# Optimization experiments

Hardware: AMD Instinct MI355X
Metric: run time of the kernel (lower is better)

The kernel has to match this reference:

```python
import jax, jax.numpy as jnp
import numpy as np

B, S, H, E, I, K = 1, 4096, 1024, 16, 512, 2
ISH = 1024  # shared expert intermediate = moe_intermediate_size * num_shared_experts
ROUTE_SCALE = 1.0
WSCALE = 0.02


def setup_inputs() -> dict:
    key = jax.random.key(0)
    ks = jax.random.split(key, 9)
    return {
        "hidden_states": jax.random.normal(ks[0], (B, S, H), dtype=jnp.float32),
        "router_w": jax.random.normal(ks[1], (H, E), dtype=jnp.float32) * WSCALE,
        "expert_bias": jnp.zeros((E,), dtype=jnp.float32),
        "w_gate": jax.random.normal(ks[2], (E, H, I), dtype=jnp.float32) * WSCALE,
        "w_up": jax.random.normal(ks[3], (E, H, I), dtype=jnp.float32) * WSCALE,
        "w_down": jax.random.normal(ks[4], (E, I, H), dtype=jnp.float32) * WSCALE,
        "sw_gate": jax.random.normal(ks[5], (H, ISH), dtype=jnp.float32) * WSCALE,
        "sw_up": jax.random.normal(ks[6], (H, ISH), dtype=jnp.float32) * WSCALE,
        "sw_down": jax.random.normal(ks[7], (ISH, H), dtype=jnp.float32) * WSCALE,
    }


def reference(hidden_states, router_w, expert_bias, w_gate, w_up, w_down, sw_gate, sw_up, sw_down):
    b, s, h = hidden_states.shape
    T = b * s
    xf = hidden_states.reshape(T, h)

    # --- token-choice router (sigmoid scores, top-k, normalize, scale) ---
    scores = jax.nn.sigmoid((xf @ router_w).astype(jnp.float32))          # [T, E]
    _, sel = jax.lax.top_k(scores + expert_bias[None, :], K)              # [T, K] int32
    top = jnp.take_along_axis(scores, sel, axis=1)                        # [T, K]
    top = top / (top.sum(axis=-1, keepdims=True) + 1e-20)
    top = top * ROUTE_SCALE

    # combine weights: [T, E], zero for unselected experts
    comb = jnp.zeros((T, E), jnp.float32).at[jnp.arange(T)[:, None], sel].add(top)

    # --- routed experts: SwiGLU MLP per expert (stacked weights) ---
    g = jnp.einsum('th,ehi->eti', xf, w_gate)                             # [E, T, I]
    u = jnp.einsum('th,ehi->eti', xf, w_up)                               # [E, T, I]
    a = jax.nn.silu(g) * u                                                # [E, T, I]
    eo = jnp.einsum('eti,eih->eth', a, w_down)                            # [E, T, H]
    routed = jnp.einsum('eth,te->th', eo.astype(jnp.float32), comb).astype(hidden_states.dtype)

    # --- shared experts (always active) ---
    shared = (jax.nn.silu(xf @ sw_gate) * (xf @ sw_up)) @ sw_down         # [T, H]

    return (shared + routed).reshape(b, s, h)
```

## Files before the change

kernel.cpp:

```cpp
#include <hip/hip_runtime.h>
#include <math.h>

#define T_TOK 4096
#define HDIM  1024
#define NEXP  16
#define IDIM  512
#define NSLOT 16384
#define NGRP  18
#define MAXRB 160

typedef unsigned int u32;
typedef unsigned short u16;
typedef __attribute__((ext_vector_type(8))) short bfrag;
typedef __attribute__((ext_vector_type(4))) float f32x4;

__device__ __forceinline__ u16 f2bf(float f) {
    union { float f; u32 u; } c; c.f = f;
    u32 u = c.u;
    u32 r = u + 0x7fffu + ((u >> 16) & 1u);
    return (u16)(r >> 16);
}
__device__ __forceinline__ float bf2f(u16 h) {
    union { u32 u; float f; } c; c.u = ((u32)h) << 16;
    return c.f;
}

__device__ __forceinline__ void async16(void* lds, const void* g) {
    __builtin_amdgcn_global_load_lds((__attribute__((address_space(1))) void*)(g),
                                     (__attribute__((address_space(3))) void*)(lds),
                                     16, 0, 0);
}

__global__ __launch_bounds__(256) void cvt_f32_bf16(const float* __restrict__ src,
                                                    u16* __restrict__ dst, int n) {
    int i = (blockIdx.x * 256 + threadIdx.x) * 4;
    if (i >= n) return;
    float4 v = *(const float4*)(src + i);
    ushort4 o;
    o.x = f2bf(v.x); o.y = f2bf(v.y); o.z = f2bf(v.z); o.w = f2bf(v.w);
    *(ushort4*)(dst + i) = o;
}

__global__ __launch_bounds__(256) void transpose_k(const float* __restrict__ src,
                                                   u16* __restrict__ dst,
                                                   int R, int C, long bstride) {
    __shared__ float tile[32][33];
    long base = (long)blockIdx.z * bstride;
    int c0 = blockIdx.x * 32, r0 = blockIdx.y * 32;
    int tx = threadIdx.x, ty = threadIdx.y;
#pragma unroll
    for (int j = 0; j < 4; ++j)
        tile[ty + 8 * j][tx] = src[base + (long)(r0 + ty + 8 * j) * C + (c0 + tx)];
    __syncthreads();
#pragma unroll
    for (int j = 0; j < 4; ++j)
        dst[base + (long)(c0 + ty + 8 * j) * R + (r0 + tx)] = f2bf(tile[tx][ty + 8 * j]);
}

__global__ __launch_bounds__(256) void router_k(const float* __restrict__ x,
                                                const float* __restrict__ rw,
                                                const float* __restrict__ bias,
                                                int* __restrict__ sel,
                                                float* __restrict__ wts) {
    int tid = threadIdx.x;
    int wv = tid >> 6;
    int lane = tid & 63;
    int t = blockIdx.x * 4 + wv;
    int e = lane & 15, hc = lane >> 4;
    const float* xr = x + (long)t * HDIM + hc * 256;
    const float* rp = rw + (long)hc * 256 * NEXP + e;
    float acc = 0.f;
#pragma unroll 4
    for (int i = 0; i < 64; ++i) {
        float4 xv = *(const float4*)(xr + i * 4);
        acc += xv.x * rp[(i * 4 + 0) * NEXP] + xv.y * rp[(i * 4 + 1) * NEXP]
             + xv.z * rp[(i * 4 + 2) * NEXP] + xv.w * rp[(i * 4 + 3) * NEXP];
    }
    acc += __shfl_down(acc, 16);
    acc += __shfl_down(acc, 32);
    float sc = 1.f / (1.f + __expf(-acc));
    float v = sc + bias[e];
    int i0 = -1, i1 = -1;
    float v0 = -1e30f, v1 = -1e30f, s0 = 0.f, s1 = 0.f;
#pragma unroll
    for (int j = 0; j < 16; ++j) {
        float vj = __shfl(v, j);
        float scj = __shfl(sc, j);
        if (vj > v0) { v1 = v0; i1 = i0; s1 = s0; v0 = vj; i0 = j; s0 = scj; }
        else if (vj > v1) { v1 = vj; i1 = j; s1 = scj; }
    }
    if (lane == 0) {
        float nrm = s0 + s1 + 1e-20f;
        sel[t * 2] = i0; sel[t * 2 + 1] = i1;
        wts[t * 2] = s0 / nrm; wts[t * 2 + 1] = s1 / nrm;
    }
}

__global__ __launch_bounds__(1024) void route_build_k(const int* __restrict__ sel,
                                                      int* __restrict__ offs,
                                                      int* __restrict__ rowmap,
                                                      int* __restrict__ invmap,
                                                      int* __restrict__ rbGroup,
                                                      int* __restrict__ rbRow0) {
    __shared__ int hist[NEXP];
    __shared__ int cur[NEXP];
    int tid = threadIdx.x;
    if (tid < NEXP) hist[tid] = 0;
    __syncthreads();
    for (int i = tid; i < T_TOK * 2; i += 1024)
        atomicAdd(&hist[sel[i]], 1);
    __syncthreads();
    if (tid == 0) {
        int a = 0;
        for (int g = 0; g < NEXP; ++g) { cur[g] = a; offs[g] = a; a += hist[g]; }
        offs[16] = 8192;
        offs[17] = 8192 + T_TOK;
        offs[18] = 8192 + 2 * T_TOK;
        int rb = 0;
        for (int g = 0; g < NGRP; ++g)
            for (int r0 = offs[g]; r0 < offs[g + 1]; r0 += 128) {
                rbGroup[rb] = g; rbRow0[rb] = r0; ++rb;
            }
        for (; rb < MAXRB; ++rb) rbGroup[rb] = -1;
    }
    __syncthreads();
    for (int i = tid; i < T_TOK * 2; i += 1024) {
        int g = sel[i];
        int slot = atomicAdd(&cur[g], 1);
        rowmap[slot] = i >> 1;
        invmap[i] = slot;
    }
    for (int i = tid; i < T_TOK; i += 1024) {
        rowmap[8192 + i] = i;
        rowmap[8192 + T_TOK + i] = i;
    }
}

__global__ __launch_bounds__(256)
void gemm_gu(const u16* __restrict__ A,
             const u16* __restrict__ WG,
             const u16* __restrict__ WU,
             const u16* __restrict__ SWG,
             const u16* __restrict__ SWU,
             u16* __restrict__ H,
             const int* __restrict__ offs,
             const int* __restrict__ rowmap,
             const int* __restrict__ rbGroup,
             const int* __restrict__ rbRow0) {
    int rb = blockIdx.y;
    int g = rbGroup[rb];
    if (g < 0) return;
    int row0 = rbRow0[rb];
    int mend = offs[g + 1];
    int col0 = blockIdx.x * 64;
    long wb = (long)((g < 16) ? g : (g - 16)) * IDIM * HDIM;
    const u16* Bg = (g < 16) ? WG + wb : SWG + wb;
    const u16* Bu = (g < 16) ? WU + wb : SWU + wb;

    __shared__ u16 sA[128 * 64];
    __shared__ u16 sBg[64 * 64];
    __shared__ u16 sBu[64 * 64];

    int tid = threadIdx.x;
    int lane = tid & 63;
    int w = tid >> 6;
    int wr = (w >> 1) * 64, wc = (w & 1) * 32;
    int lhi = lane >> 4, llo = lane & 15;
    int swz = llo & 7;

    const u16* pA[4]; u16* dA[4];
#pragma unroll
    for (int c = 0; c < 4; ++c) {
        int idx = c * 256 + tid;
        int r = idx >> 3, ch = idx & 7;
        int grow = row0 + r;
        int ar = rowmap[(grow < mend) ? grow : row0];
        pA[c] = A + (long)ar * HDIM + ((ch ^ (r & 7)) * 8);
        dA[c] = &sA[idx * 8];
    }
    const u16* pBg[2]; const u16* pBu[2]; u16* dBg[2]; u16* dBu[2];
#pragma unroll
    for (int c = 0; c < 2; ++c) {
        int idx = c * 256 + tid;
        int r = idx >> 3, ch = idx & 7;
        long boff = (long)(col0 + r) * HDIM + ((ch ^ (r & 7)) * 8);
        pBg[c] = Bg + boff; pBu[c] = Bu + boff;
        dBg[c] = &sBg[idx * 8]; dBu[c] = &sBu[idx * 8];
    }

    f32x4 accg[4][2], accu[4][2];
#pragma unroll
    for (int m = 0; m < 4; ++m)
#pragma unroll
        for (int n = 0; n < 2; ++n) {
            f32x4 z = {0.f, 0.f, 0.f, 0.f};
            accg[m][n] = z; accu[m][n] = z;
        }

    for (int k0 = 0; k0 < HDIM; k0 += 64) {
#pragma unroll
        for (int c = 0; c < 4; ++c) { async16(dA[c], pA[c]); pA[c] += 64; }
#pragma unroll
        for (int c = 0; c < 2; ++c) {
            async16(dBg[c], pBg[c]); pBg[c] += 64;
            async16(dBu[c], pBu[c]); pBu[c] += 64;
        }
        __syncthreads();
#pragma unroll
        for (int kk = 0; kk < 2; ++kk) {
            int p = ((kk * 4 + lhi) ^ swz) * 8;
            bfrag a[4], bg[2], bu[2];
#pragma unroll
            for (int m = 0; m < 4; ++m)
                a[m] = *(const bfrag*)&sA[(wr + m * 16 + llo) * 64 + p];
#pragma unroll
            for (int n = 0; n < 2; ++n) {
                bg[n] = *(const bfrag*)&sBg[(wc + n * 16 + llo) * 64 + p];
                bu[n] = *(const bfrag*)&sBu[(wc + n * 16 + llo) * 64 + p];
            }
#pragma unroll
            for (int m = 0; m < 4; ++m)
#pragma unroll
                for (int n = 0; n < 2; ++n) {
                    accg[m][n] = __builtin_amdgcn_mfma_f32_16x16x32_bf16(a[m], bg[n], accg[m][n], 0, 0, 0);
                    accu[m][n] = __builtin_amdgcn_mfma_f32_16x16x32_bf16(a[m], bu[n], accu[m][n], 0, 0, 0);
                }
        }
        __syncthreads();
    }

#pragma unroll
    for (int m = 0; m < 4; ++m) {
        int rbase = row0 + wr + m * 16 + lhi * 4;
#pragma unroll
        for (int n = 0; n < 2; ++n) {
            int col = col0 + wc + n * 16 + llo;
#pragma unroll
            for (int i = 0; i < 4; ++i) {
                int grow = rbase + i;
                if (grow >= mend) continue;
                float gv = accg[m][n][i], uv = accu[m][n][i];
                float hv = gv / (1.f + __expf(-gv)) * uv;
                H[(long)grow * IDIM + col] = f2bf(hv);
            }
        }
    }
}

__global__ __launch_bounds__(256)
void gemm_down(const u16* __restrict__ Hbuf,
               const u16* __restrict__ WD,
               const u16* __restrict__ SWD,
               u16* __restrict__ EO,
               const int* __restrict__ offs,
               const int* __restrict__ rbGroup,
               const int* __restrict__ rbRow0) {
    int rb = blockIdx.y;
    int g = rbGroup[rb];
    if (g < 0) return;
    int row0 = rbRow0[rb];
    int mend = offs[g + 1];
    int col0 = blockIdx.x * 128;
    long wb = (long)((g < 16) ? g : (g - 16)) * HDIM * IDIM;
    const u16* B = (g < 16) ? WD + wb : SWD + wb;

    __shared__ u16 sA[128 * 64];
    __shared__ u16 sB[128 * 64];

    int tid = threadIdx.x;
    int lane = tid & 63;
    int w = tid >> 6;
    int wr = (w >> 1) * 64, wc = (w & 1) * 64;
    int lhi = lane >> 4, llo = lane & 15;
    int swz = llo & 7;

    const u16* pA[4]; const u16* pB[4]; u16* dA[4]; u16* dB[4];
#pragma unroll
    for (int c = 0; c < 4; ++c) {
        int idx = c * 256 + tid;
        int r = idx >> 3, ch = idx & 7;
        int grow = row0 + r;
        int ar = (grow < mend) ? grow : row0;
        int chs = (ch ^ (r & 7)) * 8;
        pA[c] = Hbuf + (long)ar * IDIM + chs;
        pB[c] = B + (long)(col0 + r) * IDIM + chs;
        dA[c] = &sA[idx * 8];
        dB[c] = &sB[idx * 8];
    }

    f32x4 acc[4][4];
#pragma unroll
    for (int m = 0; m < 4; ++m)
#pragma unroll
        for (int n = 0; n < 4; ++n) { f32x4 z = {0.f, 0.f, 0.f, 0.f}; acc[m][n] = z; }

    for (int k0 = 0; k0 < IDIM; k0 += 64) {
#pragma unroll
        for (int c = 0; c < 4; ++c) {
            async16(dA[c], pA[c]); pA[c] += 64;
            async16(dB[c], pB[c]); pB[c] += 64;
        }
        __syncthreads();
#pragma unroll
        for (int kk = 0; kk < 2; ++kk) {
            int p = ((kk * 4 + lhi) ^ swz) * 8;
            bfrag a[4], b[4];
#pragma unroll
            for (int m = 0; m < 4; ++m)
                a[m] = *(const bfrag*)&sA[(wr + m * 16 + llo) * 64 + p];
#pragma unroll
            for (int n = 0; n < 4; ++n)
                b[n] = *(const bfrag*)&sB[(wc + n * 16 + llo) * 64 + p];
#pragma unroll
            for (int m = 0; m < 4; ++m)
#pragma unroll
                for (int n = 0; n < 4; ++n)
                    acc[m][n] = __builtin_amdgcn_mfma_f32_16x16x32_bf16(a[m], b[n], acc[m][n], 0, 0, 0);
        }
        __syncthreads();
    }

#pragma unroll
    for (int m = 0; m < 4; ++m) {
        int rbase = row0 + wr + m * 16 + lhi * 4;
#pragma unroll
        for (int n = 0; n < 4; ++n) {
            int col = col0 + wc + n * 16 + llo;
#pragma unroll
            for (int i = 0; i < 4; ++i) {
                int grow = rbase + i;
                if (grow >= mend) continue;
                EO[(long)grow * HDIM + col] = f2bf(acc[m][n][i]);
            }
        }
    }
}

__global__ __launch_bounds__(256) void combine_k(float* __restrict__ out,
                                                 const u16* __restrict__ eo,
                                                 const int* __restrict__ invmap,
                                                 const float* __restrict__ wts) {
    int t = blockIdx.x;
    int h = threadIdx.x * 4;
    int r0 = invmap[t * 2], r1 = invmap[t * 2 + 1];
    float w0 = wts[t * 2], w1 = wts[t * 2 + 1];
    int s0 = 8192 + t, s1 = 8192 + T_TOK + t;
    ushort4 a = *(const ushort4*)(eo + (long)r0 * HDIM + h);
    ushort4 b = *(const ushort4*)(eo + (long)r1 * HDIM + h);
    ushort4 c = *(const ushort4*)(eo + (long)s0 * HDIM + h);
    ushort4 d = *(const ushort4*)(eo + (long)s1 * HDIM + h);
    float4 o;
    o.x = w0 * bf2f(a.x) + w1 * bf2f(b.x) + bf2f(c.x) + bf2f(d.x);
    o.y = w0 * bf2f(a.y) + w1 * bf2f(b.y) + bf2f(c.y) + bf2f(d.y);
    o.z = w0 * bf2f(a.z) + w1 * bf2f(b.z) + bf2f(c.z) + bf2f(d.z);
    o.w = w0 * bf2f(a.w) + w1 * bf2f(b.w) + bf2f(c.w) + bf2f(d.w);
    *(float4*)(out + (long)t * HDIM + h) = o;
}

extern "C" void kernel_launch(void* const* d_in, const int* in_sizes, int n_in,
                              void* d_out, int out_size, void* d_ws, size_t ws_size,
                              hipStream_t stream) {
    const float* x    = (const float*)d_in[0];
    const float* rw   = (const float*)d_in[1];
    const float* bias = (const float*)d_in[2];
    const float* wg   = (const float*)d_in[3];
    const float* wu   = (const float*)d_in[4];
    const float* wd   = (const float*)d_in[5];
    const float* swg  = (const float*)d_in[6];
    const float* swu  = (const float*)d_in[7];
    const float* swd  = (const float*)d_in[8];
    float* out = (float*)d_out;

    char* ws = (char*)d_ws;
    size_t o = 0;
    auto alloc = [&](size_t bytes) -> void* {
        void* p = ws + o;
        o += (bytes + 255) & ~(size_t)255;
        return p;
    };
    u16* x_bf = (u16*)alloc((size_t)T_TOK * HDIM * 2);
    u16* WtG  = (u16*)alloc((size_t)NEXP * IDIM * HDIM * 2);
    u16* WtU  = (u16*)alloc((size_t)NEXP * IDIM * HDIM * 2);
    u16* WtD  = (u16*)alloc((size_t)NEXP * HDIM * IDIM * 2);
    u16* SWtG = (u16*)alloc((size_t)2 * IDIM * HDIM * 2);
    u16* SWtU = (u16*)alloc((size_t)2 * IDIM * HDIM * 2);
    u16* SWtD = (u16*)alloc((size_t)2 * HDIM * IDIM * 2);
    u16* Hbuf = (u16*)alloc((size_t)NSLOT * IDIM * 2);
    int*   sel     = (int*)alloc((size_t)T_TOK * 2 * 4);
    float* wts     = (float*)alloc((size_t)T_TOK * 2 * 4);
    int*   invmap  = (int*)alloc((size_t)T_TOK * 2 * 4);
    int*   rowmap  = (int*)alloc((size_t)NSLOT * 4);
    int*   offs    = (int*)alloc((NGRP + 1) * 4);
    int*   rbGroup = (int*)alloc(MAXRB * 4);
    int*   rbRow0  = (int*)alloc(MAXRB * 4);
    u16* EO = WtG;

    cvt_f32_bf16<<<dim3((T_TOK * HDIM) / (4 * 256)), 256, 0, stream>>>(x, x_bf, T_TOK * HDIM);

    transpose_k<<<dim3(IDIM / 32, HDIM / 32, NEXP), dim3(32, 8), 0, stream>>>(wg, WtG, HDIM, IDIM, (long)HDIM * IDIM);
    transpose_k<<<dim3(IDIM / 32, HDIM / 32, NEXP), dim3(32, 8), 0, stream>>>(wu, WtU, HDIM, IDIM, (long)HDIM * IDIM);
    transpose_k<<<dim3(HDIM / 32, IDIM / 32, NEXP), dim3(32, 8), 0, stream>>>(wd, WtD, IDIM, HDIM, (long)IDIM * HDIM);
    transpose_k<<<dim3(32, 32, 1), dim3(32, 8), 0, stream>>>(swg, SWtG, HDIM, 2 * IDIM, 0);
    transpose_k<<<dim3(32, 32, 1), dim3(32, 8), 0, stream>>>(swu, SWtU, HDIM, 2 * IDIM, 0);
    transpose_k<<<dim3(HDIM / 32, IDIM / 32, 2), dim3(32, 8), 0, stream>>>(swd, SWtD, IDIM, HDIM, (long)IDIM * HDIM);

    router_k<<<dim3(T_TOK / 4), 256, 0, stream>>>(x, rw, bias, sel, wts);
    route_build_k<<<dim3(1), 1024, 0, stream>>>(sel, offs, rowmap, invmap, rbGroup, rbRow0);

    gemm_gu<<<dim3(IDIM / 64, MAXRB), 256, 0, stream>>>(
        x_bf, WtG, WtU, SWtG, SWtU, Hbuf, offs, rowmap, rbGroup, rbRow0);

    gemm_down<<<dim3(HDIM / 128, MAXRB), 256, 0, stream>>>(
        Hbuf, WtD, SWtD, EO, offs, rbGroup, rbRow0);

    combine_k<<<dim3(T_TOK), 256, 0, stream>>>(out, EO, invmap, wts);
}
```

Baseline: 176.0 us.

## Double-buffer LDS tiles in gate/up and down GEMMs with async prefetch

Both grouped GEMM kernels now keep two LDS buffers and issue the global-to-LDS loads for the next K tile before computing the current one. They wait on a partial vmcnt so the prefetch stays in flight during the MFMAs, instead of fully syncing on every tile. This doubles LDS usage per block, which may reduce occupancy. It also relies on hand-counted vmcnt values and a hardcoded trip count.

```diff
diff --git a/kernel.cpp b/kernel.cpp
--- a/kernel.cpp
+++ b/kernel.cpp
@@ -30,6 +30,16 @@
                                      (__attribute__((address_space(3))) void*)(lds),
                                      16, 0, 0);
 }
+
+#define SYNCN(n) do { \
+    asm volatile("s_waitcnt vmcnt(" #n ")" ::: "memory"); \
+    __builtin_amdgcn_s_barrier(); \
+    __builtin_amdgcn_sched_barrier(0); \
+} while (0)
+#define BAR2() do { \
+    __builtin_amdgcn_s_barrier(); \
+    __builtin_amdgcn_sched_barrier(0); \
+} while (0)
 
 __global__ __launch_bounds__(256) void cvt_f32_bf16(const float* __restrict__ src,
                                                     u16* __restrict__ dst, int n) {
@@ -157,9 +167,9 @@
     const u16* Bg = (g < 16) ? WG + wb : SWG + wb;
     const u16* Bu = (g < 16) ? WU + wb : SWU + wb;
 
-    __shared__ u16 sA[128 * 64];
-    __shared__ u16 sBg[64 * 64];
-    __shared__ u16 sBu[64 * 64];
+    __shared__ u16 sA[2][128 * 64];
+    __shared__ u16 sBg[2][64 * 64];
+    __shared__ u16 sBu[2][64 * 64];
 
     int tid = threadIdx.x;
     int lane = tid & 63;
@@ -168,7 +178,7 @@
     int lhi = lane >> 4, llo = lane & 15;
     int swz = llo & 7;
 
-    const u16* pA[4]; u16* dA[4];
+    const u16* pA[4]; int dA[4];
 #pragma unroll
     for (int c = 0; c < 4; ++c) {
         int idx = c * 256 + tid;
@@ -176,16 +186,16 @@
         int grow = row0 + r;
         int ar = rowmap[(grow < mend) ? grow : row0];
         pA[c] = A + (long)ar * HDIM + ((ch ^ (r & 7)) * 8);
-        dA[c] = &sA[idx * 8];
-    }
-    const u16* pBg[2]; const u16* pBu[2]; u16* dBg[2]; u16* dBu[2];
+        dA[c] = idx * 8;
+    }
+    const u16* pBg[2]; const u16* pBu[2]; int dB[2];
 #pragma unroll
     for (int c = 0; c < 2; ++c) {
         int idx = c * 256 + tid;
         int r = idx >> 3, ch = idx & 7;
         long boff = (long)(col0 + r) * HDIM + ((ch ^ (r & 7)) * 8);
         pBg[c] = Bg + boff; pBu[c] = Bu + boff;
-        dBg[c] = &sBg[idx * 8]; dBu[c] = &sBu[idx * 8];
+        dB[c] = idx * 8;
     }
 
     f32x4 accg[4][2], accu[4][2];
@@ -197,26 +207,27 @@
             accg[m][n] = z; accu[m][n] = z;
         }
 
-    for (int k0 = 0; k0 < HDIM; k0 += 64) {
-#pragma unroll
-        for (int c = 0; c < 4; ++c) { async16(dA[c], pA[c]); pA[c] += 64; }
+    auto STAGE = [&](int buf) {
+#pragma unroll
+        for (int c = 0; c < 4; ++c) { async16(&sA[buf][dA[c]], pA[c]); pA[c] += 64; }
 #pragma unroll
         for (int c = 0; c < 2; ++c) {
-            async16(dBg[c], pBg[c]); pBg[c] += 64;
-            async16(dBu[c], pBu[c]); pBu[c] += 64;
-        }
-        __syncthreads();
+            async16(&sBg[buf][dB[c]], pBg[c]); pBg[c] += 64;
+            async16(&sBu[buf][dB[c]], pBu[c]); pBu[c] += 64;
+        }
+    };
+    auto COMPUTE = [&](int buf) {
 #pragma unroll
         for (int kk = 0; kk < 2; ++kk) {
             int p = ((kk * 4 + lhi) ^ swz) * 8;
             bfrag a[4], bg[2], bu[2];
 #pragma unroll
             for (int m = 0; m < 4; ++m)
-                a[m] = *(const bfrag*)&sA[(wr + m * 16 + llo) * 64 + p];
+                a[m] = *(const bfrag*)&sA[buf][(wr + m * 16 + llo) * 64 + p];
 #pragma unroll
             for (int n = 0; n < 2; ++n) {
-                bg[n] = *(const bfrag*)&sBg[(wc + n * 16 + llo) * 64 + p];
-                bu[n] = *(const bfrag*)&sBu[(wc + n * 16 + llo) * 64 + p];
+                bg[n] = *(const bfrag*)&sBg[buf][(wc + n * 16 + llo) * 64 + p];
+                bu[n] = *(const bfrag*)&sBu[buf][(wc + n * 16 + llo) * 64 + p];
             }
 #pragma unroll
             for (int m = 0; m < 4; ++m)
@@ -226,8 +237,16 @@
                     accu[m][n] = __builtin_amdgcn_mfma_f32_16x16x32_bf16(a[m], bu[n], accu[m][n], 0, 0, 0);
                 }
         }
-        __syncthreads();
-    }
+    };
+
+    STAGE(0);
+#pragma unroll 1
+    for (int t = 0; t < 14; t += 2) {
+        STAGE(1); SYNCN(8); COMPUTE(0); BAR2();
+        STAGE(0); SYNCN(8); COMPUTE(1); BAR2();
+    }
+    STAGE(1); SYNCN(8); COMPUTE(0); BAR2();
+    SYNCN(0); COMPUTE(1);
 
 #pragma unroll
     for (int m = 0; m < 4; ++m) {
@@ -264,8 +283,8 @@
     long wb = (long)((g < 16) ? g : (g - 16)) * HDIM * IDIM;
     const u16* B = (g < 16) ? WD + wb : SWD + wb;
 
-    __shared__ u16 sA[128 * 64];
-    __shared__ u16 sB[128 * 64];
+    __shared__ u16 sA[2][128 * 64];
+    __shared__ u16 sB[2][128 * 64];
 
     int tid = threadIdx.x;
     int lane = tid & 63;
@@ -274,7 +293,7 @@
     int lhi = lane >> 4, llo = lane & 15;
     int swz = llo & 7;
 
-    const u16* pA[4]; const u16* pB[4]; u16* dA[4]; u16* dB[4];
+    const u16* pA[4]; const u16* pB[4]; int dd[4];
 #pragma unroll
     for (int c = 0; c < 4; ++c) {
         int idx = c * 256 + tid;
@@ -284,8 +303,7 @@
         int chs = (ch ^ (r & 7)) * 8;
         pA[c] = Hbuf + (long)ar * IDIM + chs;
         pB[c] = B + (long)(col0 + r) * IDIM + chs;
-        dA[c] = &sA[idx * 8];
-        dB[c] = &sB[idx * 8];
+        dd[c] = idx * 8;
     }
 
     f32x4 acc[4][4];
@@ -294,31 +312,40 @@
 #pragma unroll
         for (int n = 0; n < 4; ++n) { f32x4 z = {0.f, 0.f, 0.f, 0.f}; acc[m][n] = z; }
 
-    for (int k0 = 0; k0 < IDIM; k0 += 64) {
+    auto STAGE = [&](int buf) {
 #pragma unroll
         for (int c = 0; c < 4; ++c) {
-            async16(dA[c], pA[c]); pA[c] += 64;
-            async16(dB[c], pB[c]); pB[c] += 64;
-        }
-        __syncthreads();
+            async16(&sA[buf][dd[c]], pA[c]); pA[c] += 64;
+            async16(&sB[buf][dd[c]], pB[c]); pB[c] += 64;
+        }
+    };
+    auto COMPUTE = [&](int buf) {
 #pragma unroll
         for (int kk = 0; kk < 2; ++kk) {
             int p = ((kk * 4 + lhi) ^ swz) * 8;
             bfrag a[4], b[4];
 #pragma unroll
             for (int m = 0; m < 4; ++m)
-                a[m] = *(const bfrag*)&sA[(wr + m * 16 + llo) * 64 + p];
+                a[m] = *(const bfrag*)&sA[buf][(wr + m * 16 + llo) * 64 + p];
 #pragma unroll
             for (int n = 0; n < 4; ++n)
-                b[n] = *(const bfrag*)&sB[(wc + n * 16 + llo) * 64 + p];
+                b[n] = *(const bfrag*)&sB[buf][(wc + n * 16 + llo) * 64 + p];
 #pragma unroll
             for (int m = 0; m < 4; ++m)
 #pragma unroll
                 for (int n = 0; n < 4; ++n)
                     acc[m][n] = __builtin_amdgcn_mfma_f32_16x16x32_bf16(a[m], b[n], acc[m][n], 0, 0, 0);
         }
-        __syncthreads();
-    }
+    };
+
+    STAGE(0);
+#pragma unroll 1
+    for (int t = 0; t < 6; t += 2) {
+        STAGE(1); SYNCN(8); COMPUTE(0); BAR2();
+        STAGE(0); SYNCN(8); COMPUTE(1); BAR2();
+    }
+    STAGE(1); SYNCN(8); COMPUTE(0); BAR2();
+    SYNCN(0); COMPUTE(1);
 
 #pragma unroll
     for (int m = 0; m < 4; ++m) {
```

New measurement: 175.7 us. About the same (-0.2%).
